# Kernel tuning notes

Hardware: AMD Instinct MI355X
Metric: run time of the kernel (lower is better)

## Reference

```python
import jax, jax.numpy as jnp
import numpy as np

B, N, FEA = 4, 200000, 9
G = 32                      # per-axis index range used for voxel keys
NUM_SEG = B * G * G * G     # 131072 = max possible unique voxels (static)
OUT_DIM, COMPRE = 256, 16
BN_EPS = 1e-5

def _glorot(k, shape):
    lim = float(np.sqrt(6.0 / (shape[0] + shape[1])))
    return jax.random.uniform(k, shape, jnp.float32, -lim, lim)

def setup_inputs() -> dict:
    key = jax.random.key(0)
    ks = jax.random.split(key, 16)
    inp = {
        "pt_fea": jax.random.normal(ks[0], (B, N, FEA), jnp.float32),
        "xy_ind": jax.random.randint(ks[1], (B, N, 3), 0, G, dtype=jnp.int32),
    }
    dims = [FEA, 64, 128, 256, OUT_DIM]
    bn_dims = [FEA, 64, 128, 256]
    for i, d in enumerate(bn_dims):
        inp[f"bn{i}_g"] = jnp.ones((d,), jnp.float32)
        inp[f"bn{i}_b"] = jnp.zeros((d,), jnp.float32)
        inp[f"bn{i}_m"] = jax.random.normal(ks[2 + i], (d,), jnp.float32) * 0.1
        inp[f"bn{i}_v"] = jnp.ones((d,), jnp.float32)
    for i in range(4):
        inp[f"w{i+1}"] = _glorot(ks[6 + i], (dims[i], dims[i + 1]))
        inp[f"b{i+1}"] = jnp.zeros((dims[i + 1],), jnp.float32)
    inp["wc"] = _glorot(ks[10], (OUT_DIM, COMPRE))
    inp["bc"] = jnp.zeros((COMPRE,), jnp.float32)
    return inp

def _bn(x, g, b, m, v):
    return (x - m) * jax.lax.rsqrt(v + BN_EPS) * g + b

def reference(pt_fea, xy_ind, bn0_g, bn0_b, bn0_m, bn0_v,
              bn1_g, bn1_b, bn1_m, bn1_v, bn2_g, bn2_b, bn2_m, bn2_v,
              bn3_g, bn3_b, bn3_m, bn3_v,
              w1, b1, w2, b2, w3, b3, w4, b4, wc, bc):
    # flatten batched point clouds; build scalar voxel key = (batch, ix, iy, iz)
    b_idx = jnp.broadcast_to(jnp.arange(B, dtype=jnp.int32)[:, None], (B, N)).reshape(-1)
    ind = xy_ind.reshape(B * N, 3)
    keys = ((b_idx * G + ind[:, 0]) * G + ind[:, 1]) * G + ind[:, 2]  # [B*N]
    fea = pt_fea.reshape(B * N, FEA)

    # torch.unique(dim=0) equivalent: sorted unique keys + inverse map (static size)
    unq_keys, unq_inv = jnp.unique(keys, size=NUM_SEG, fill_value=-1, return_inverse=True)

    # torch_scatter.scatter_max over voxels
    pooled = jax.ops.segment_max(fea, unq_inv, num_segments=NUM_SEG)
    cnt = jax.ops.segment_sum(jnp.ones((B * N,), jnp.float32), unq_inv, num_segments=NUM_SEG)
    pooled = jnp.where(cnt[:, None] > 0, pooled, 0.0)  # neutralize empty padding slots (-inf)

    # PPmodel: BN -> Linear -> BN -> ReLU (x3) -> Linear (eval-mode BatchNorm)
    x = _bn(pooled, bn0_g, bn0_b, bn0_m, bn0_v)
    x = jax.nn.relu(_bn(x @ w1 + b1, bn1_g, bn1_b, bn1_m, bn1_v))
    x = jax.nn.relu(_bn(x @ w2 + b2, bn2_g, bn2_b, bn2_m, bn2_v))
    x = jax.nn.relu(_bn(x @ w3 + b3, bn3_g, bn3_b, bn3_m, bn3_v))
    x = x @ w4 + b4
    out = jax.nn.relu(x @ wc + bc)  # fea_compression

    # decode keys back to [num_vox, 4] int64 (batch, ix, iy, iz); padding rows = -1
    valid = unq_keys >= 0
    kk = jnp.where(valid, unq_keys, 0)
    unq = jnp.stack([kk // (G * G * G), (kk // (G * G)) % G, (kk // G) % G, kk % G], axis=1)
    unq = jnp.where(valid[:, None], unq, -1)
    return unq.astype(jnp.int64), out
```

## Files before the change

### kernel.cpp

```cpp
#include <hip/hip_runtime.h>

#define NPTS   800000
#define NPB    200000
#define NSEG   131072
#define OUT_OFF (NSEG*4)
#define BN_EPS 1e-5f
#define BCAP   3072
#define KC_PTS 2048
#define KC_CAP 32

typedef __attribute__((ext_vector_type(8))) __bf16 bf16x8;
typedef __attribute__((ext_vector_type(4))) float  f32x4;

#define MFMA16 __builtin_amdgcn_mfma_f32_16x16x32_bf16

__device__ __forceinline__ unsigned short f2bf(float f) {
    unsigned u = __float_as_uint(f);
    u += 0x7fffu + ((u >> 16) & 1u);
    return (unsigned short)(u >> 16);
}
__device__ __forceinline__ unsigned encf(float f) {
    unsigned u = __float_as_uint(f);
    return (u & 0x80000000u) ? ~u : (u | 0x80000000u);
}
__device__ __forceinline__ float decf(unsigned e) {
    unsigned u = (e & 0x80000000u) ? (e & 0x7FFFFFFFu) : ~e;
    return __uint_as_float(u);
}

__global__ void k_fold(const float* __restrict__ g0, const float* __restrict__ be0,
                       const float* __restrict__ m0, const float* __restrict__ v0,
                       const float* __restrict__ g1, const float* __restrict__ be1,
                       const float* __restrict__ m1, const float* __restrict__ v1,
                       const float* __restrict__ g2, const float* __restrict__ be2,
                       const float* __restrict__ m2, const float* __restrict__ v2,
                       const float* __restrict__ g3, const float* __restrict__ be3,
                       const float* __restrict__ m3, const float* __restrict__ v3,
                       const float* __restrict__ w1, const float* __restrict__ b1,
                       const float* __restrict__ w2, const float* __restrict__ b2,
                       const float* __restrict__ w3, const float* __restrict__ b3,
                       const float* __restrict__ w4, const float* __restrict__ b4,
                       const float* __restrict__ wc, const float* __restrict__ bc,
                       unsigned short* __restrict__ WT1, float* __restrict__ c1,
                       unsigned short* __restrict__ WT2, float* __restrict__ c2,
                       unsigned short* __restrict__ WT3, float* __restrict__ c3,
                       unsigned short* __restrict__ WT4, float* __restrict__ c4,
                       unsigned* __restrict__ bucketFill) {
    int id = blockIdx.x * 256 + threadIdx.x;
    if (id < 32768) {
        int j = id >> 7, k = id & 127;
        float s = g3[j] * rsqrtf(v3[j] + BN_EPS);
        WT3[id] = f2bf(w3[k*256 + j] * s);
    } else if (id < 40960) {
        int t = id - 32768; int j = t >> 6, k = t & 63;
        float s = g2[j] * rsqrtf(v2[j] + BN_EPS);
        WT2[t] = f2bf(w2[k*128 + j] * s);
    } else if (id < 45056) {
        int t = id - 40960; int j = t >> 8, k = t & 255;
        float acc = 0.f;
        for (int i = 0; i < 256; ++i) acc += w4[k*256 + i] * wc[i*16 + j];
        WT4[t] = f2bf(acc);
    } else if (id < 47104) {
        int t = id - 45056; int j = t >> 5, k = t & 31;
        float val = 0.f;
        if (k < 9) {
            float s0 = g0[k] * rsqrtf(v0[k] + BN_EPS);
            float s1 = g1[j] * rsqrtf(v1[j] + BN_EPS);
            val = s0 * w1[k*64 + j] * s1;
        }
        WT1[t] = f2bf(val);
    } else if (id < 47168) {
        int j = id - 47104;
        float s1 = g1[j] * rsqrtf(v1[j] + BN_EPS);
        float acc = b1[j];
        for (int k = 0; k < 9; ++k) {
            float s0 = g0[k] * rsqrtf(v0[k] + BN_EPS);
            float t0 = be0[k] - m0[k] * s0;
            acc += t0 * w1[k*64 + j];
        }
        c1[j] = (acc - m1[j]) * s1 + be1[j];
    } else if (id < 47296) {
        int j = id - 47168;
        float s = g2[j] * rsqrtf(v2[j] + BN_EPS);
        c2[j] = (b2[j] - m2[j]) * s + be2[j];
    } else if (id < 47552) {
        int j = id - 47296;
        float s = g3[j] * rsqrtf(v3[j] + BN_EPS);
        c3[j] = (b3[j] - m3[j]) * s + be3[j];
    } else if (id < 47568) {
        int j = id - 47552;
        float acc = bc[j];
        for (int i = 0; i < 256; ++i) acc += b4[i] * wc[i*16 + j];
        c4[j] = acc;
    } else if (id < 48080) {
        bucketFill[id - 47568] = 0u;
    }
}

__global__ void __launch_bounds__(512)
kC(const int* __restrict__ ind, unsigned* __restrict__ bucketFill,
   unsigned* __restrict__ bucketed) {
    __shared__ unsigned lh[256], gb[256];
    __shared__ unsigned stash[256*KC_CAP];
    const int t = threadIdx.x;
    const int base = blockIdx.x * KC_PTS;
    const int b0 = base / NPB;
    if (t < 256) lh[t] = 0u;
    __syncthreads();
    int loc[4]; unsigned slot[4]; unsigned pay[4];
    #pragma unroll
    for (int i = 0; i < 4; ++i) {
        int p = base + i*512 + t;
        if (p < NPTS) {
            int ix = ind[p*3], iy = ind[p*3+1], iz = ind[p*3+2];
            int b = p / NPB;
            loc[i] = (b - b0)*128 + ix*4 + (iy >> 3);
            pay[i] = ((unsigned)((iy & 7)*32 + iz) << 20) | (unsigned)p;
            slot[i] = atomicAdd(&lh[loc[i]], 1u);
            if (slot[i] < KC_CAP) stash[loc[i]*KC_CAP + slot[i]] = pay[i];
        } else loc[i] = -1;
    }
    __syncthreads();
    if (t < 256 && lh[t] > 0u) gb[t] = atomicAdd(&bucketFill[b0*128 + t], lh[t]);
    __syncthreads();
    for (int i = t; i < 256*KC_CAP; i += 512) {
        int s = i >> 5, e = i & (KC_CAP-1);
        unsigned n = lh[s]; if (n > KC_CAP) n = KC_CAP;
        if ((unsigned)e < n) {
            unsigned pos = gb[s] + (unsigned)e;
            if (pos < BCAP) bucketed[(size_t)(b0*128 + s)*BCAP + pos] = stash[i];
        }
    }
    #pragma unroll
    for (int i = 0; i < 4; ++i) if (loc[i] >= 0 && slot[i] >= KC_CAP) {
        unsigned pos = gb[loc[i]] + slot[i];
        if (pos < BCAP) bucketed[(size_t)(b0*128 + loc[i])*BCAP + pos] = pay[i];
    }
}

__global__ void __launch_bounds__(1024)
kD(const float* __restrict__ fea,
   const unsigned* __restrict__ bucketFill, const unsigned* __restrict__ bucketed,
   float* __restrict__ pooledD, unsigned long long* __restrict__ occW) {
    __shared__ unsigned enc[256*9];
    const int t = threadIdx.x, bkt = blockIdx.x;
    for (int i = t; i < 2304; i += 1024) enc[i] = 0u;
    __syncthreads();
    unsigned n = bucketFill[bkt]; if (n > BCAP) n = BCAP;
    for (unsigned j = t; j < n; j += 1024) {
        unsigned e = bucketed[bkt*BCAP + j];
        unsigned p = e & 0xFFFFFu;
        unsigned v = e >> 20;
        const float* fp = fea + (size_t)p*9;
        float4 q0 = *reinterpret_cast<const float4*>(fp);
        float4 q1 = *reinterpret_cast<const float4*>(fp + 4);
        float  f8 = fp[8];
        unsigned* eb = enc + v*9;
        atomicMax(eb+0, encf(q0.x)); atomicMax(eb+1, encf(q0.y));
        atomicMax(eb+2, encf(q0.z)); atomicMax(eb+3, encf(q0.w));
        atomicMax(eb+4, encf(q1.x)); atomicMax(eb+5, encf(q1.y));
        atomicMax(eb+6, encf(q1.z)); atomicMax(eb+7, encf(q1.w));
        atomicMax(eb+8, encf(f8));
    }
    __syncthreads();
    if (t < 256) {
        int occ = (enc[t*9] != 0u) ? 1 : 0;
        unsigned long long m = __ballot(occ);
        if ((t & 63) == 0) occW[bkt*4 + (t >> 6)] = m;
    }
    for (int e = t; e < 2304; e += 1024) {
        int v = e / 9;
        float val = (enc[v*9] != 0u) ? decf(enc[e]) : 0.f;
        pooledD[(size_t)(bkt*256 + v)*9 + (e - v*9)] = val;
    }
}

__global__ void kScan(const unsigned long long* __restrict__ occW,
                      unsigned* __restrict__ wordBase, unsigned* __restrict__ totSlot) {
    __shared__ unsigned s[512];
    const int t = threadIdx.x;
    unsigned c[4], sum = 0u;
    #pragma unroll
    for (int i = 0; i < 4; ++i) { c[i] = (unsigned)__popcll(occW[t*4+i]); sum += c[i]; }
    s[t] = sum;
    __syncthreads();
    for (int off = 1; off < 512; off <<= 1) {
        unsigned add = (t >= off) ? s[t-off] : 0u;
        __syncthreads();
        s[t] += add;
        __syncthreads();
    }
    unsigned run = s[t] - sum;
    #pragma unroll
    for (int i = 0; i < 4; ++i) { wordBase[t*4+i] = run; run += c[i]; }
    if (t == 511) totSlot[0] = s[511];
}


__device__ __forceinline__ void store4(char* base, int r, int strideElems, int n, f32x4 acc) {
    union { __bf16 h[4]; uint2 u; } pk;
    #pragma unroll
    for (int i = 0; i < 4; ++i) pk.h[i] = (__bf16)fmaxf(acc[i], 0.f);
    int s = n >> 3;
    *reinterpret_cast<uint2*>(base + r*strideElems*2 + ((s ^ (r & 7)) << 4) + (n & 4)*2) = pk.u;
}

__global__ void __launch_bounds__(512, 2)
k_mlp(const float* __restrict__ pooledD,
      const unsigned long long* __restrict__ occW,
      const unsigned* __restrict__ wordBase,
      const unsigned* __restrict__ totSlot,
      const unsigned short* __restrict__ WT1, const float* __restrict__ c1,
      const unsigned short* __restrict__ WT2, const float* __restrict__ c2,
      const unsigned short* __restrict__ WT3, const float* __restrict__ c3,
      const unsigned short* __restrict__ WT4, const float* __restrict__ c4,
      float* __restrict__ unqOut, float* __restrict__ outF) {
    __shared__ __align__(16) char lds[61440];
    char* Rin = lds;
    char* H1  = lds + 4096;
    char* H2  = lds + 12288;
    char* H3  = lds + 28672;
    const int tid = threadIdx.x;
    const int wv = tid >> 6, lane = tid & 63;
    const int r16 = lane & 15, kg = lane >> 4;

    for (int i = tid; i < 1024; i += 512) reinterpret_cast<unsigned*>(Rin)[i] = 0u;

    const int ft1 = wv & 3;
    bf16x8 a1 = *reinterpret_cast<const bf16x8*>(WT1 + (ft1*16 + r16)*32 + kg*8);
    f32x4 c1v = *reinterpret_cast<const f32x4*>(c1 + ft1*16 + kg*4);
    bf16x8 a2[2];
    #pragma unroll
    for (int ks = 0; ks < 2; ++ks)
        a2[ks] = *reinterpret_cast<const bf16x8*>(WT2 + (wv*16 + r16)*64 + ks*32 + kg*8);
    f32x4 c2v = *reinterpret_cast<const f32x4*>(c2 + wv*16 + kg*4);
    bf16x8 a3[2][4]; f32x4 c3v[2];
    #pragma unroll
    for (int u = 0; u < 2; ++u) {
        int ft = wv*2 + u;
        #pragma unroll
        for (int ks = 0; ks < 4; ++ks)
            a3[u][ks] = *reinterpret_cast<const bf16x8*>(WT3 + (ft*16 + r16)*128 + ks*32 + kg*8);
        c3v[u] = *reinterpret_cast<const f32x4*>(c3 + ft*16 + kg*4);
    }
    bf16x8 a4[8]; f32x4 c4v;
    if (wv < 4) {
        #pragma unroll
        for (int ks = 0; ks < 8; ++ks)
            a4[ks] = *reinterpret_cast<const bf16x8*>(WT4 + r16*256 + ks*32 + kg*8);
        c4v = *reinterpret_cast<const f32x4*>(c4 + kg*4);
    }
    const unsigned tot = totSlot[0];
    __syncthreads();

    int tile = blockIdx.x;
    float pf0, pf1;
    {
        const float* src = pooledD + (size_t)tile * 576;
        pf0 = src[tid];
        pf1 = (tid < 64) ? src[512 + tid] : 0.f;
    }
    #pragma unroll 1
    for (int it = 0; it < 8; ++it) {
        {
            int r = tid / 9, c = tid - r*9;
            *reinterpret_cast<__bf16*>(Rin + r*64 + (((c>>3) ^ (r&3))<<4) + (c&7)*2) = (__bf16)pf0;
            if (tid < 64) {
                int j = 512 + tid; int r2 = j / 9, c2 = j - r2*9;
                *reinterpret_cast<__bf16*>(Rin + r2*64 + (((c2>>3) ^ (r2&3))<<4) + (c2&7)*2) = (__bf16)pf1;
            }
        }
        unsigned long long w = occW[tile];
        unsigned base = wordBase[tile];
        if (it < 7) {
            const float* src = pooledD + ((size_t)tile + 256) * 576;
            pf0 = src[tid];
            if (tid < 64) pf1 = src[512 + tid];
        }
        __syncthreads();
        {
            const int rtb = (wv >> 2) * 2;
            #pragma unroll
            for (int i = 0; i < 2; ++i) {
                int r = (rtb + i)*16 + r16;
                bf16x8 b = *reinterpret_cast<const bf16x8*>(Rin + r*64 + ((kg ^ (r&3))<<4));
                f32x4 acc = MFMA16(a1, b, c1v, 0, 0, 0);
                store4(H1, r, 64, ft1*16 + kg*4, acc);
            }
        }
        __syncthreads();
        #pragma unroll
        for (int rt = 0; rt < 4; ++rt) {
            int r = rt*16 + r16;
            bf16x8 b0 = *reinterpret_cast<const bf16x8*>(H1 + r*128 + ((kg ^ (r&7))<<4));
            bf16x8 b1 = *reinterpret_cast<const bf16x8*>(H1 + r*128 + (((4+kg) ^ (r&7))<<4));
            f32x4 acc = MFMA16(a2[0], b0, c2v, 0, 0, 0);
            acc = MFMA16(a2[1], b1, acc, 0, 0, 0);
            store4(H2, r, 128, wv*16 + kg*4, acc);
        }
        __syncthreads();
        #pragma unroll
        for (int rt = 0; rt < 4; ++rt) {
            int r = rt*16 + r16;
            bf16x8 b[4];
            #pragma unroll
            for (int ks = 0; ks < 4; ++ks)
                b[ks] = *reinterpret_cast<const bf16x8*>(H2 + r*256 + (((ks*4+kg) ^ (r&7))<<4));
            #pragma unroll
            for (int u = 0; u < 2; ++u) {
                f32x4 acc = c3v[u];
                #pragma unroll
                for (int ks = 0; ks < 4; ++ks)
                    acc = MFMA16(a3[u][ks], b[ks], acc, 0, 0, 0);
                store4(H3, r, 256, (wv*2+u)*16 + kg*4, acc);
            }
        }
        __syncthreads();
        if (wv < 4) {
            int r = wv*16 + r16;
            f32x4 acc = c4v;
            #pragma unroll
            for (int ks = 0; ks < 8; ++ks) {
                bf16x8 b = *reinterpret_cast<const bf16x8*>(H3 + r*512 + (((ks*4+kg) ^ (r&7))<<4));
                acc = MFMA16(a4[ks], b, acc, 0, 0, 0);
            }
            unsigned rdense = base + (unsigned)__popcll(w & ((1ull << r) - 1ull));
            unsigned rk = ((w >> r) & 1ull) ? rdense
                        : tot + (unsigned)(tile*64 + r) - rdense;
            float4 o;
            o.x = fmaxf(acc[0], 0.f); o.y = fmaxf(acc[1], 0.f);
            o.z = fmaxf(acc[2], 0.f); o.w = fmaxf(acc[3], 0.f);
            *reinterpret_cast<float4*>(outF + (size_t)rk*16 + kg*4) = o;
        } else if (wv == 4) {
            int r = lane, k = tile*64 + r;
            unsigned rdense = base + (unsigned)__popcll(w & ((1ull << r) - 1ull));
            if ((w >> r) & 1ull) {
                reinterpret_cast<float4*>(unqOut)[rdense] =
                    make_float4((float)(k >> 15), (float)((k >> 10) & 31),
                                (float)((k >> 5) & 31), (float)(k & 31));
            } else {
                unsigned er = tot + (unsigned)k - rdense;
                reinterpret_cast<float4*>(unqOut)[er] = make_float4(-1.f,-1.f,-1.f,-1.f);
            }
        }
        tile += 256;
    }
}

extern "C" void kernel_launch(void* const* d_in, const int* in_sizes, int n_in,
                              void* d_out, int out_size, void* d_ws, size_t ws_size,
                              hipStream_t stream) {
    const float* pt_fea = (const float*)d_in[0];
    const int*   xy_ind = (const int*)  d_in[1];
    const float* g0 = (const float*)d_in[2],  *be0 = (const float*)d_in[3];
    const float* m0 = (const float*)d_in[4],  *v0  = (const float*)d_in[5];
    const float* g1 = (const float*)d_in[6],  *be1 = (const float*)d_in[7];
    const float* m1 = (const float*)d_in[8],  *v1  = (const float*)d_in[9];
    const float* g2 = (const float*)d_in[10], *be2 = (const float*)d_in[11];
    const float* m2 = (const float*)d_in[12], *v2  = (const float*)d_in[13];
    const float* g3 = (const float*)d_in[14], *be3 = (const float*)d_in[15];
    const float* m3 = (const float*)d_in[16], *v3  = (const float*)d_in[17];
    const float* w1 = (const float*)d_in[18], *b1  = (const float*)d_in[19];
    const float* w2 = (const float*)d_in[20], *b2  = (const float*)d_in[21];
    const float* w3 = (const float*)d_in[22], *b3  = (const float*)d_in[23];
    const float* w4 = (const float*)d_in[24], *b4  = (const float*)d_in[25];
    const float* wc = (const float*)d_in[26], *bc  = (const float*)d_in[27];

    float* dout = (float*)d_out;

    unsigned* ws0 = (unsigned*)d_ws;
    unsigned long long* occW = (unsigned long long*)ws0;
    unsigned* bucketFill = ws0 + 4096;
    unsigned* wordBase   = ws0 + 4608;
    unsigned* totSlot    = ws0 + 6656;
    unsigned* bucketed   = ws0 + 6672;
    float*    pooledD    = (float*)(bucketed + 512*BCAP);
    unsigned short* WT1  = (unsigned short*)(pooledD + (size_t)NSEG*9);
    unsigned short* WT2  = WT1 + 2048;
    unsigned short* WT3  = WT2 + 8192;
    unsigned short* WT4  = WT3 + 32768;
    float* c1 = (float*)(WT4 + 4096);
    float* c2 = c1 + 64;
    float* c3 = c2 + 128;
    float* c4 = c3 + 256;

    k_fold<<<188, 256, 0, stream>>>(g0,be0,m0,v0, g1,be1,m1,v1, g2,be2,m2,v2, g3,be3,m3,v3,
                                    w1,b1, w2,b2, w3,b3, w4,b4, wc,bc,
                                    WT1,c1, WT2,c2, WT3,c3, WT4,c4, bucketFill);
    kC<<<(NPTS + KC_PTS - 1)/KC_PTS, 512, 0, stream>>>(xy_ind, bucketFill, bucketed);
    kD<<<512, 1024, 0, stream>>>(pt_fea, bucketFill, bucketed, pooledD, occW);
    kScan<<<1, 512, 0, stream>>>(occW, wordBase, totSlot);
    k_mlp<<<256, 512, 0, stream>>>(pooledD, occW, wordBase, totSlot,
                                   WT1,c1, WT2,c2, WT3,c3, WT4,c4, dout, dout + OUT_OFF);
}
```

Baseline: 69.08 us.

## Read features in bucketing pass, pack bf16 payloads, fuse scan into MLP

The bucketing kernel now reads point features directly, converts them to sortable bf16, and writes them as five coalesced payload planes. The pooling kernel then does contiguous plane reads instead of random gathers into the feature array. The pooled output is stored as packed bf16 pairs, which halves the traffic into the MLP kernel. The separate scan kernel is removed and each MLP block recomputes the occupancy prefix sum itself. This cuts one launch and the random feature gathers, at the cost of redundant scans and reduced precision when taking the max over bf16 values, which was already applied at MLP input. Bucket capacity is reduced to 2048, and each block now processes 1600 points with a 24-entry stash per bucket.

After: 63.07 us. -8.7%, faster.

```diff
diff --git a/kernel.cpp b/kernel.cpp
--- a/kernel.cpp
+++ b/kernel.cpp
@@ -5,9 +5,8 @@
 #define NSEG   131072
 #define OUT_OFF (NSEG*4)
 #define BN_EPS 1e-5f
-#define BCAP   3072
-#define KC_PTS 2048
-#define KC_CAP 32
+#define BCAP   2048
+#define PLANE  (512*BCAP)
 
 typedef __attribute__((ext_vector_type(8))) __bf16 bf16x8;
 typedef __attribute__((ext_vector_type(4))) float  f32x4;
@@ -19,13 +18,11 @@
     u += 0x7fffu + ((u >> 16) & 1u);
     return (unsigned short)(u >> 16);
 }
-__device__ __forceinline__ unsigned encf(float f) {
-    unsigned u = __float_as_uint(f);
-    return (u & 0x80000000u) ? ~u : (u | 0x80000000u);
-}
-__device__ __forceinline__ float decf(unsigned e) {
-    unsigned u = (e & 0x80000000u) ? (e & 0x7FFFFFFFu) : ~e;
-    return __uint_as_float(u);
+__device__ __forceinline__ unsigned enc16(unsigned short b) {
+    return (b & 0x8000u) ? ((~(unsigned)b) & 0xFFFFu) : ((unsigned)b | 0x8000u);
+}
+__device__ __forceinline__ unsigned dec16(unsigned e) {
+    return (e >= 0x8000u) ? (e & 0x7FFFu) : ((~e) & 0xFFFFu);
 }
 
 __global__ void k_fold(const float* __restrict__ g0, const float* __restrict__ be0,
@@ -98,69 +95,92 @@
 }
 
 __global__ void __launch_bounds__(512)
-kC(const int* __restrict__ ind, unsigned* __restrict__ bucketFill,
-   unsigned* __restrict__ bucketed) {
-    __shared__ unsigned lh[256], gb[256];
-    __shared__ unsigned stash[256*KC_CAP];
+kC(const int* __restrict__ ind, const float* __restrict__ fea,
+   unsigned* __restrict__ bucketFill, unsigned* __restrict__ bP) {
+    __shared__ unsigned lh[128], gb[128];
+    __shared__ unsigned stash[5][128*24];
     const int t = threadIdx.x;
-    const int base = blockIdx.x * KC_PTS;
+    const int base = blockIdx.x * 1600;
     const int b0 = base / NPB;
-    if (t < 256) lh[t] = 0u;
-    __syncthreads();
-    int loc[4]; unsigned slot[4]; unsigned pay[4];
+    if (t < 128) lh[t] = 0u;
+    __syncthreads();
+    int loc[4]; unsigned slot[4]; unsigned pw[4][5];
     #pragma unroll
     for (int i = 0; i < 4; ++i) {
-        int p = base + i*512 + t;
-        if (p < NPTS) {
+        int pl = i*512 + t;
+        if (pl < 1600) {
+            int p = base + pl;
             int ix = ind[p*3], iy = ind[p*3+1], iz = ind[p*3+2];
-            int b = p / NPB;
-            loc[i] = (b - b0)*128 + ix*4 + (iy >> 3);
-            pay[i] = ((unsigned)((iy & 7)*32 + iz) << 20) | (unsigned)p;
+            loc[i] = ix*4 + (iy >> 3);
+            unsigned v = (unsigned)((iy & 7)*32 + iz);
+            const float* fp = fea + (size_t)p*9;
+            float4 q0 = *reinterpret_cast<const float4*>(fp);
+            float4 q1 = *reinterpret_cast<const float4*>(fp + 4);
+            float  f8 = fp[8];
+            unsigned e0 = enc16(f2bf(q0.x)), e1 = enc16(f2bf(q0.y));
+            unsigned e2 = enc16(f2bf(q0.z)), e3 = enc16(f2bf(q0.w));
+            unsigned e4 = enc16(f2bf(q1.x)), e5 = enc16(f2bf(q1.y));
+            unsigned e6 = enc16(f2bf(q1.z)), e7 = enc16(f2bf(q1.w));
+            unsigned e8 = enc16(f2bf(f8));
+            pw[i][0] = (v << 16) | e0;
+            pw[i][1] = e1 | (e2 << 16);
+            pw[i][2] = e3 | (e4 << 16);
+            pw[i][3] = e5 | (e6 << 16);
+            pw[i][4] = e7 | (e8 << 16);
             slot[i] = atomicAdd(&lh[loc[i]], 1u);
-            if (slot[i] < KC_CAP) stash[loc[i]*KC_CAP + slot[i]] = pay[i];
+            if (slot[i] < 24u) {
+                #pragma unroll
+                for (int w = 0; w < 5; ++w) stash[w][loc[i]*24 + slot[i]] = pw[i][w];
+            }
         } else loc[i] = -1;
     }
     __syncthreads();
-    if (t < 256 && lh[t] > 0u) gb[t] = atomicAdd(&bucketFill[b0*128 + t], lh[t]);
-    __syncthreads();
-    for (int i = t; i < 256*KC_CAP; i += 512) {
-        int s = i >> 5, e = i & (KC_CAP-1);
-        unsigned n = lh[s]; if (n > KC_CAP) n = KC_CAP;
+    if (t < 128 && lh[t] > 0u) gb[t] = atomicAdd(&bucketFill[b0*128 + t], lh[t]);
+    __syncthreads();
+    for (int idx = t; idx < 128*24; idx += 512) {
+        int s = idx / 24, e = idx - s*24;
+        unsigned n = lh[s]; if (n > 24u) n = 24u;
         if ((unsigned)e < n) {
             unsigned pos = gb[s] + (unsigned)e;
-            if (pos < BCAP) bucketed[(size_t)(b0*128 + s)*BCAP + pos] = stash[i];
-        }
-    }
-    #pragma unroll
-    for (int i = 0; i < 4; ++i) if (loc[i] >= 0 && slot[i] >= KC_CAP) {
+            if (pos < BCAP) {
+                size_t off = (size_t)(b0*128 + s)*BCAP + pos;
+                #pragma unroll
+                for (int w = 0; w < 5; ++w) bP[(size_t)w*PLANE + off] = stash[w][idx];
+            }
+        }
+    }
+    #pragma unroll
+    for (int i = 0; i < 4; ++i) if (loc[i] >= 0 && slot[i] >= 24u) {
         unsigned pos = gb[loc[i]] + slot[i];
-        if (pos < BCAP) bucketed[(size_t)(b0*128 + loc[i])*BCAP + pos] = pay[i];
+        if (pos < BCAP) {
+            size_t off = (size_t)(b0*128 + loc[i])*BCAP + pos;
+            #pragma unroll
+            for (int w = 0; w < 5; ++w) bP[(size_t)w*PLANE + off] = pw[i][w];
+        }
     }
 }
 
 __global__ void __launch_bounds__(1024)
-kD(const float* __restrict__ fea,
-   const unsigned* __restrict__ bucketFill, const unsigned* __restrict__ bucketed,
-   float* __restrict__ pooledD, unsigned long long* __restrict__ occW) {
+kD(const unsigned* __restrict__ bucketFill, const unsigned* __restrict__ bP,
+   unsigned* __restrict__ pooledB, unsigned long long* __restrict__ occW) {
     __shared__ unsigned enc[256*9];
     const int t = threadIdx.x, bkt = blockIdx.x;
     for (int i = t; i < 2304; i += 1024) enc[i] = 0u;
     __syncthreads();
     unsigned n = bucketFill[bkt]; if (n > BCAP) n = BCAP;
     for (unsigned j = t; j < n; j += 1024) {
-        unsigned e = bucketed[bkt*BCAP + j];
-        unsigned p = e & 0xFFFFFu;
-        unsigned v = e >> 20;
-        const float* fp = fea + (size_t)p*9;
-        float4 q0 = *reinterpret_cast<const float4*>(fp);
-        float4 q1 = *reinterpret_cast<const float4*>(fp + 4);
-        float  f8 = fp[8];
-        unsigned* eb = enc + v*9;
-        atomicMax(eb+0, encf(q0.x)); atomicMax(eb+1, encf(q0.y));
-        atomicMax(eb+2, encf(q0.z)); atomicMax(eb+3, encf(q0.w));
-        atomicMax(eb+4, encf(q1.x)); atomicMax(eb+5, encf(q1.y));
-        atomicMax(eb+6, encf(q1.z)); atomicMax(eb+7, encf(q1.w));
-        atomicMax(eb+8, encf(f8));
+        size_t off = (size_t)bkt*BCAP + j;
+        unsigned w0 = bP[off];
+        unsigned w1 = bP[PLANE + off];
+        unsigned w2 = bP[2*(size_t)PLANE + off];
+        unsigned w3 = bP[3*(size_t)PLANE + off];
+        unsigned w4 = bP[4*(size_t)PLANE + off];
+        unsigned* eb = enc + (w0 >> 16)*9;
+        atomicMax(eb+0, w0 & 0xFFFFu);
+        atomicMax(eb+1, w1 & 0xFFFFu); atomicMax(eb+2, w1 >> 16);
+        atomicMax(eb+3, w2 & 0xFFFFu); atomicMax(eb+4, w2 >> 16);
+        atomicMax(eb+5, w3 & 0xFFFFu); atomicMax(eb+6, w3 >> 16);
+        atomicMax(eb+7, w4 & 0xFFFFu); atomicMax(eb+8, w4 >> 16);
     }
     __syncthreads();
     if (t < 256) {
@@ -168,32 +188,13 @@
         unsigned long long m = __ballot(occ);
         if ((t & 63) == 0) occW[bkt*4 + (t >> 6)] = m;
     }
-    for (int e = t; e < 2304; e += 1024) {
-        int v = e / 9;
-        float val = (enc[v*9] != 0u) ? decf(enc[e]) : 0.f;
-        pooledD[(size_t)(bkt*256 + v)*9 + (e - v*9)] = val;
-    }
-}
-
-__global__ void kScan(const unsigned long long* __restrict__ occW,
-                      unsigned* __restrict__ wordBase, unsigned* __restrict__ totSlot) {
-    __shared__ unsigned s[512];
-    const int t = threadIdx.x;
-    unsigned c[4], sum = 0u;
-    #pragma unroll
-    for (int i = 0; i < 4; ++i) { c[i] = (unsigned)__popcll(occW[t*4+i]); sum += c[i]; }
-    s[t] = sum;
-    __syncthreads();
-    for (int off = 1; off < 512; off <<= 1) {
-        unsigned add = (t >= off) ? s[t-off] : 0u;
-        __syncthreads();
-        s[t] += add;
-        __syncthreads();
-    }
-    unsigned run = s[t] - sum;
-    #pragma unroll
-    for (int i = 0; i < 4; ++i) { wordBase[t*4+i] = run; run += c[i]; }
-    if (t == 511) totSlot[0] = s[511];
+    for (int e2 = t; e2 < 1152; e2 += 1024) {
+        int ea = 2*e2, eb2 = ea + 1;
+        int va = ea / 9, vb = eb2 / 9;
+        unsigned da = enc[va*9] ? dec16(enc[ea])  : 0u;
+        unsigned db = enc[vb*9] ? dec16(enc[eb2]) : 0u;
+        pooledB[(size_t)bkt*1152 + e2] = da | (db << 16);
+    }
 }
 
 
@@ -206,10 +207,8 @@
 }
 
 __global__ void __launch_bounds__(512, 2)
-k_mlp(const float* __restrict__ pooledD,
+k_mlp(const unsigned* __restrict__ pooledB,
       const unsigned long long* __restrict__ occW,
-      const unsigned* __restrict__ wordBase,
-      const unsigned* __restrict__ totSlot,
       const unsigned short* __restrict__ WT1, const float* __restrict__ c1,
       const unsigned short* __restrict__ WT2, const float* __restrict__ c2,
       const unsigned short* __restrict__ WT3, const float* __restrict__ c3,
@@ -250,33 +249,58 @@
             a4[ks] = *reinterpret_cast<const bf16x8*>(WT4 + r16*256 + ks*32 + kg*8);
         c4v = *reinterpret_cast<const f32x4*>(c4 + kg*4);
     }
-    const unsigned tot = totSlot[0];
+
+    unsigned* sS  = reinterpret_cast<unsigned*>(H3);
+    unsigned* wbS = reinterpret_cast<unsigned*>(H3 + 2048);
+    unsigned pc0 = (unsigned)__popcll(occW[tid*4+0]);
+    unsigned pc1 = (unsigned)__popcll(occW[tid*4+1]);
+    unsigned pc2 = (unsigned)__popcll(occW[tid*4+2]);
+    unsigned pc3 = (unsigned)__popcll(occW[tid*4+3]);
+    unsigned psum = pc0 + pc1 + pc2 + pc3;
+    sS[tid] = psum;
+    __syncthreads();
+    for (int off = 1; off < 512; off <<= 1) {
+        unsigned add = (tid >= off) ? sS[tid-off] : 0u;
+        __syncthreads();
+        sS[tid] += add;
+        __syncthreads();
+    }
+    unsigned ex = sS[tid] - psum;
+    const unsigned tot = sS[511];
+    #pragma unroll
+    for (int k = 0; k < 8; ++k) {
+        int tl = blockIdx.x + 256*k;
+        if (tid == (tl >> 2)) {
+            unsigned b = ex; int o = tl & 3;
+            if (o > 0) b += pc0;
+            if (o > 1) b += pc1;
+            if (o > 2) b += pc2;
+            wbS[k] = b;
+        }
+    }
+    __syncthreads();
+    unsigned wb[8];
+    #pragma unroll
+    for (int k = 0; k < 8; ++k) wb[k] = wbS[k];
     __syncthreads();
 
     int tile = blockIdx.x;
-    float pf0, pf1;
-    {
-        const float* src = pooledD + (size_t)tile * 576;
-        pf0 = src[tid];
-        pf1 = (tid < 64) ? src[512 + tid] : 0.f;
-    }
+    unsigned pf;
+    if (tid < 288) pf = pooledB[(size_t)tile*288 + tid];
     #pragma unroll 1
     for (int it = 0; it < 8; ++it) {
-        {
-            int r = tid / 9, c = tid - r*9;
-            *reinterpret_cast<__bf16*>(Rin + r*64 + (((c>>3) ^ (r&3))<<4) + (c&7)*2) = (__bf16)pf0;
-            if (tid < 64) {
-                int j = 512 + tid; int r2 = j / 9, c2 = j - r2*9;
-                *reinterpret_cast<__bf16*>(Rin + r2*64 + (((c2>>3) ^ (r2&3))<<4) + (c2&7)*2) = (__bf16)pf1;
-            }
+        if (tid < 288) {
+            int ea = 2*tid, eb = ea + 1;
+            int ra = ea / 9, ca = ea - ra*9;
+            int rb = eb / 9, cb = eb - rb*9;
+            *reinterpret_cast<unsigned short*>(Rin + ra*64 + (((ca>>3) ^ (ra&3))<<4) + (ca&7)*2)
+                = (unsigned short)(pf & 0xFFFFu);
+            *reinterpret_cast<unsigned short*>(Rin + rb*64 + (((cb>>3) ^ (rb&3))<<4) + (cb&7)*2)
+                = (unsigned short)(pf >> 16);
         }
         unsigned long long w = occW[tile];
-        unsigned base = wordBase[tile];
-        if (it < 7) {
-            const float* src = pooledD + ((size_t)tile + 256) * 576;
-            pf0 = src[tid];
-            if (tid < 64) pf1 = src[512 + tid];
-        }
+        unsigned base = wb[it];
+        if (it < 7 && tid < 288) pf = pooledB[((size_t)tile + 256)*288 + tid];
         __syncthreads();
         {
             const int rtb = (wv >> 2) * 2;
@@ -371,11 +395,10 @@
     unsigned* ws0 = (unsigned*)d_ws;
     unsigned long long* occW = (unsigned long long*)ws0;
     unsigned* bucketFill = ws0 + 4096;
-    unsigned* wordBase   = ws0 + 4608;
-    unsigned* totSlot    = ws0 + 6656;
-    unsigned* bucketed   = ws0 + 6672;
-    float*    pooledD    = (float*)(bucketed + 512*BCAP);
-    unsigned short* WT1  = (unsigned short*)(pooledD + (size_t)NSEG*9);
+    unsigned* pooledB    = ws0 + 4608;
+    unsigned* bP         = pooledB + 512*1152;
+    unsigned* wtBase     = bP + 5*(size_t)PLANE;
+    unsigned short* WT1  = (unsigned short*)wtBase;
     unsigned short* WT2  = WT1 + 2048;
     unsigned short* WT3  = WT2 + 8192;
     unsigned short* WT4  = WT3 + 32768;
@@ -387,9 +410,8 @@
     k_fold<<<188, 256, 0, stream>>>(g0,be0,m0,v0, g1,be1,m1,v1, g2,be2,m2,v2, g3,be3,m3,v3,
                                     w1,b1, w2,b2, w3,b3, w4,b4, wc,bc,
                                     WT1,c1, WT2,c2, WT3,c3, WT4,c4, bucketFill);
-    kC<<<(NPTS + KC_PTS - 1)/KC_PTS, 512, 0, stream>>>(xy_ind, bucketFill, bucketed);
-    kD<<<512, 1024, 0, stream>>>(pt_fea, bucketFill, bucketed, pooledD, occW);
-    kScan<<<1, 512, 0, stream>>>(occW, wordBase, totSlot);
-    k_mlp<<<256, 512, 0, stream>>>(pooledD, occW, wordBase, totSlot,
+    kC<<<500, 512, 0, stream>>>(xy_ind, pt_fea, bucketFill, bP);
+    kD<<<512, 1024, 0, stream>>>(bucketFill, bP, pooledB, occW);
+    k_mlp<<<256, 512, 0, stream>>>(pooledB, occW,
                                    WT1,c1, WT2,c2, WT3,c3, WT4,c4, dout, dout + OUT_OFF);
 }
```
